# Optimization experiments

Hardware: AMD Instinct MI355X
Metric: run time of the kernel (lower is better)

The kernel has to match this reference:

```python
import jax, jax.numpy as jnp
import numpy as np

MARGIN = 70.0
THR = 125.0
PD_EPS = 1e-6  # torch F.pairwise_distance default eps


def _return_cam(features, weight_softmax, class_idx):
    # features: [bz, nc, h, w]; weight_softmax: [n_cls, nc]; class_idx: [bz]
    w_sel = weight_softmax[class_idx]                     # [bz, nc]
    cam = jnp.einsum('bc,bchw->bhw', w_sel, features)     # [bz, h, w]
    cam = cam - cam.min(axis=(1, 2), keepdims=True)
    cam = cam / cam.max(axis=(1, 2), keepdims=True) * 255.0
    return cam[:, None]                                   # [bz, 1, h, w]


def _pairwise_distance(x, y):
    # torch F.pairwise_distance: ||x - y + eps||_2 along last dim
    return jnp.sqrt(jnp.sum((x - y + PD_EPS) ** 2, axis=-1))


def setup_inputs() -> dict:
    key = jax.random.key(0)
    ks = jax.random.split(key, 6)
    bz, nc, h, w, n_cls = 64, 2048, 14, 14, 1000
    return {
        'pred': jax.random.normal(ks[0], (bz, n_cls), jnp.float32),
        'cla_truth': jax.random.randint(ks[1], (bz,), 0, n_cls, jnp.int32),
        'seg_truth': jax.random.uniform(ks[2], (bz, h, w), jnp.float32),
        'features_blobs': jax.random.normal(ks[3], (bz, nc, h, w), jnp.float32),
        'weight_softmax': jax.random.normal(ks[4], (n_cls, nc), jnp.float32),
        'idx': jax.random.randint(ks[5], (bz, 3), 0, n_cls, jnp.int32),
    }


def reference(pred, cla_truth, seg_truth, features_blobs, weight_softmax, idx):
    bz, nc, h, w = features_blobs.shape
    # cross entropy
    logp = jax.nn.log_softmax(pred, axis=-1)
    loss1 = -jnp.mean(logp[jnp.arange(bz), cla_truth])
    # CAMs for top-3 predicted classes
    cam0 = _return_cam(features_blobs, weight_softmax, idx[:, 0])  # [bz,1,h,w]
    cam1 = _return_cam(features_blobs, weight_softmax, idx[:, 1])
    cam2 = _return_cam(features_blobs, weight_softmax, idx[:, 2])
    # binarize cam0 (values in [0,255]); <=thr -> 0, >thr -> 1
    dst = jnp.where(cam0[:, 0] > THR, 1.0, 0.0)                     # [bz,h,w]
    # row-wise distance to seg truth, averaged over rows
    ed1 = jnp.mean(_pairwise_distance(dst, seg_truth), axis=1)      # [bz]
    # CAM-weighted features via broadcasted matmul (requires h == w)
    fea0 = jnp.matmul(cam0, features_blobs)                         # [bz,nc,h,w]
    fea1 = jnp.matmul(cam1, features_blobs)
    fea2 = jnp.matmul(cam2, features_blobs)
    d01 = _pairwise_distance(fea0.reshape(bz, -1), fea1.reshape(bz, -1)) / nc
    d02 = _pairwise_distance(fea0.reshape(bz, -1), fea2.reshape(bz, -1)) / nc
    loss_dis = jnp.mean(ed1 + jnp.clip(MARGIN - d01 - d02, 0.0, None)) + loss1
    return loss_dis
```

## Files before the change

kernel.cpp:

```cpp
#include <hip/hip_runtime.h>
#include <hip/hip_bf16.h>
#include <math.h>

#define BZ      64
#define NC      2048
#define HH      14
#define HW      196
#define NCLS    1000
#define SPLITS  8
#define CPB     (NC/SPLITS)
#define CHUNK   8
#define NCHUNK  (CPB/CHUNK)

#define CAM_OFF  0
#define G_OFF    (BZ*SPLITS*3*HW)
#define S_OFF    (G_OFF + BZ*SPLITS*HW)
#define TERM_OFF (S_OFF + BZ*SPLITS*HH)

__global__ __launch_bounds__(320) void k_stage1(
    const float* __restrict__ F, const float* __restrict__ W,
    const int* __restrict__ idx, float* __restrict__ ws)
{
  __shared__ __align__(16) float Fs[2][CHUNK*HW];
  __shared__ __align__(16) float wls[3][CPB];
  __shared__ __align__(16) float sred[HW];
  __shared__ __align__(16) float gred[224*4];

  const int t = threadIdx.x;
  const int s = blockIdx.x;
  const int b = blockIdx.y;
  const int cbase = s*CPB;

  const int i0 = idx[b*3+0], i1 = idx[b*3+1], i2 = idx[b*3+2];
  if (t < CPB){
    wls[0][t] = W[(size_t)i0*NC + cbase + t];
    wls[1][t] = W[(size_t)i1*NC + cbase + t];
    wls[2][t] = W[(size_t)i2*NC + cbase + t];
  }

  const float* Fb = F + ((size_t)b*NC + cbase)*HW;

  const bool isCam = (t < 49);
  const bool isG   = (t >= 64 && t < 288);
  int m0=0,m1=0,n0=0,n1=0, cg=0, tmKeep=0, tnKeep=0;
  if (isG){
    int g = t - 64;
    int tile = g % 28; cg = g / 28;
    int k = tile, tm = 0;
    while (k >= 7 - tm){ k -= 7 - tm; tm++; }
    int tn = tm + k;
    tmKeep = tm; tnKeep = tn;
    m0 = 2*tm; m1 = m0+1; n0 = 2*tn; n1 = n0+1;
  }
  (void)tmKeep; (void)tnKeep;

  float4 c0a = make_float4(0.f,0.f,0.f,0.f);
  float4 c1a = make_float4(0.f,0.f,0.f,0.f);
  float4 c2a = make_float4(0.f,0.f,0.f,0.f);
  float4 sA  = make_float4(0.f,0.f,0.f,0.f);
  float g00=0.f, g01=0.f, g10=0.f, g11=0.f;

  float4 pre0 = make_float4(0.f,0.f,0.f,0.f);
  float4 pre1 = make_float4(0.f,0.f,0.f,0.f);

  auto loadChunk = [&](int ch){
    if (t < 196){
      const float4* src = (const float4*)(Fb + (size_t)ch*CHUNK*HW);
      pre0 = src[2*t]; pre1 = src[2*t+1];
    }
  };
  auto storeChunk = [&](int bufi){
    if (t < 196){
      float4* dst = (float4*)(&Fs[bufi][0]);
      dst[2*t] = pre0; dst[2*t+1] = pre1;
    }
  };

  loadChunk(0);
  storeChunk(0);
  __syncthreads();

  for (int ch = 0; ch < NCHUNK; ++ch){
    const int bufi = ch & 1;
    if (ch+1 < NCHUNK) loadChunk(ch+1);
    const float* Fsb = &Fs[bufi][0];

    if (isCam){
      float w0a[CHUNK], w1a[CHUNK], w2a[CHUNK];
      *(float4*)&w0a[0] = *(const float4*)&wls[0][ch*CHUNK];
      *(float4*)&w0a[4] = *(const float4*)&wls[0][ch*CHUNK+4];
      *(float4*)&w1a[0] = *(const float4*)&wls[1][ch*CHUNK];
      *(float4*)&w1a[4] = *(const float4*)&wls[1][ch*CHUNK+4];
      *(float4*)&w2a[0] = *(const float4*)&wls[2][ch*CHUNK];
      *(float4*)&w2a[4] = *(const float4*)&wls[2][ch*CHUNK+4];
      #pragma unroll
      for (int c=0;c<CHUNK;c++){
        float4 v = *(const float4*)(Fsb + c*HW + 4*t);
        c0a.x += w0a[c]*v.x; c0a.y += w0a[c]*v.y; c0a.z += w0a[c]*v.z; c0a.w += w0a[c]*v.w;
        c1a.x += w1a[c]*v.x; c1a.y += w1a[c]*v.y; c1a.z += w1a[c]*v.z; c1a.w += w1a[c]*v.w;
        c2a.x += w2a[c]*v.x; c2a.y += w2a[c]*v.y; c2a.z += w2a[c]*v.z; c2a.w += w2a[c]*v.w;
        sA.x += v.x; sA.y += v.y; sA.z += v.z; sA.w += v.w;
      }
    }
    if (isG){
      const float* Mb = Fsb + cg*HW;
      const float2* r0 = (const float2*)(Mb + m0*HH);
      const float2* r1 = (const float2*)(Mb + m1*HH);
      const float2* q0 = (const float2*)(Mb + n0*HH);
      const float2* q1 = (const float2*)(Mb + n1*HH);
      #pragma unroll
      for (int jj=0;jj<7;jj++){
        float2 a0=r0[jj], a1=r1[jj], b0=q0[jj], b1=q1[jj];
        g00 += a0.x*b0.x + a0.y*b0.y;
        g01 += a0.x*b1.x + a0.y*b1.y;
        g10 += a1.x*b0.x + a1.y*b0.y;
        g11 += a1.x*b1.x + a1.y*b1.y;
      }
    }
    if (ch+1 < NCHUNK) storeChunk((ch+1)&1);
    __syncthreads();
  }

  const size_t pslot = (size_t)(b*SPLITS + s);
  if (isCam){
    float* base = ws + CAM_OFF + pslot*3*HW;
    *(float4*)(base          + 4*t) = c0a;
    *(float4*)(base + HW     + 4*t) = c1a;
    *(float4*)(base + 2*HW   + 4*t) = c2a;
    *(float4*)(sred + 4*t) = sA;
  }
  if (isG){
    int g = t - 64;
    float* gr = &gred[g*4];
    gr[0]=g00; gr[1]=g01; gr[2]=g10; gr[3]=g11;
  }
  __syncthreads();

  if (t < HH){
    float acc=0.f;
    #pragma unroll
    for (int j=0;j<HH;j++) acc += sred[t*HH+j];
    ws[S_OFF + pslot*HH + t] = acc;
  }
  if (t < 112){
    int tile = t >> 2, q = t & 3;
    int k = tile, tm2 = 0;
    while (k >= 7 - tm2){ k -= 7 - tm2; tm2++; }
    int tn2 = tm2 + k;
    float acc=0.f;
    #pragma unroll
    for (int c=0;c<8;c++) acc += gred[(c*28+tile)*4 + q];
    int a = q>>1, bb = q&1;
    int mm = 2*tm2 + a, nn = 2*tn2 + bb;
    float* gb = ws + G_OFF + pslot*HW;
    gb[mm*HH+nn] = acc;
    if (tn2 > tm2) gb[nn*HH+mm] = acc;
  }
}

template<int MODE>
__device__ __forceinline__ float bred(float v, float* red){
  #pragma unroll
  for (int o=32;o>0;o>>=1){
    float u = __shfl_down(v, o, 64);
    if (MODE==0) v += u; else if (MODE==1) v = fminf(v,u); else v = fmaxf(v,u);
  }
  __syncthreads();
  if ((threadIdx.x & 63)==0) red[threadIdx.x>>6] = v;
  __syncthreads();
  float r = red[0];
  #pragma unroll
  for (int w=1;w<4;w++){
    float u = red[w];
    if (MODE==0) r += u; else if (MODE==1) r = fminf(r,u); else r = fmaxf(r,u);
  }
  return r;
}

__global__ __launch_bounds__(256) void k_stage2(
    const float* __restrict__ pred, const int* __restrict__ cla,
    const float* __restrict__ seg, float* __restrict__ ws)
{
  const int t = threadIdx.x, b = blockIdx.x;
  __shared__ float cam[3][HW], Gm[HW], Sv[HH];
  __shared__ float D1[HW], D2[HW], EE[HW];
  __shared__ float rowv[HH], dc1[HH], dc2[HH];
  __shared__ float red[4];
  __shared__ float scal[6];

  if (t < HW){
    for (int k=0;k<3;k++){
      float a=0.f;
      for (int s=0;s<SPLITS;s++)
        a += ws[CAM_OFF + ((size_t)(b*SPLITS+s)*3 + k)*HW + t];
      cam[k][t]=a;
    }
    float g=0.f;
    for (int s=0;s<SPLITS;s++) g += ws[G_OFF + (size_t)(b*SPLITS+s)*HW + t];
    Gm[t]=g;
  }
  if (t < HH){
    float a=0.f;
    for (int s=0;s<SPLITS;s++) a += ws[S_OFF + (size_t)(b*SPLITS+s)*HH + t];
    Sv[t]=a;
  }
  __syncthreads();

  for (int k=0;k<3;k++){
    float v = (t<HW)? cam[k][t] : 3.0e38f;
    float mn = bred<1>(v, red);
    v = (t<HW)? cam[k][t] : -3.0e38f;
    float mx = bred<2>(v, red);
    if (t==0){ scal[2*k]=mn; scal[2*k+1]=mx; }
  }
  __syncthreads();

  if (t < HW){
    float c0 = (cam[0][t]-scal[0]) / (scal[1]-scal[0]) * 255.0f;
    float c1 = (cam[1][t]-scal[2]) / (scal[3]-scal[2]) * 255.0f;
    float c2 = (cam[2][t]-scal[4]) / (scal[5]-scal[4]) * 255.0f;
    float dst = (c0 > 125.0f) ? 1.0f : 0.0f;
    D1[t] = c0 - c1; D2[t] = c0 - c2;
    float e = dst - seg[(size_t)b*HW + t] + 1e-6f;
    EE[t] = e*e;
  }
  __syncthreads();

  if (t < HH){
    float rs=0.f, d1=0.f, d2=0.f;
    #pragma unroll
    for (int j=0;j<HH;j++){
      rs += EE[t*HH+j];
      d1 += D1[j*HH+t];
      d2 += D2[j*HH+t];
    }
    rowv[t] = sqrtf(rs); dc1[t]=d1; dc2[t]=d2;
  }
  __syncthreads();

  float v1=0.f, v2=0.f;
  if (t < HW){
    int m = t/HH, mp = t%HH;
    float h1=0.f, h2=0.f;
    #pragma unroll
    for (int i=0;i<HH;i++){
      h1 += D1[i*HH+m]*D1[i*HH+mp];
      h2 += D2[i*HH+m]*D2[i*HH+mp];
    }
    v1 = h1*Gm[t]; v2 = h2*Gm[t];
  }
  float sx2_1 = bred<0>(v1, red);
  float sx2_2 = bred<0>(v2, red);

  const float* pb = pred + (size_t)b*NCLS;
  float mv = -3.0e38f;
  for (int i=t;i<NCLS;i+=256) mv = fmaxf(mv, pb[i]);
  mv = bred<2>(mv, red);
  float es = 0.f;
  for (int i=t;i<NCLS;i+=256) es += expf(pb[i]-mv);
  es = bred<0>(es, red);

  if (t==0){
    float lse = mv + logf(es);
    float ce  = lse - pb[cla[b]];
    float ed1 = 0.f;
    #pragma unroll
    for (int i=0;i<HH;i++) ed1 += rowv[i];
    ed1 *= (1.0f/14.0f);
    float sx1=0.f, sx2=0.f;
    #pragma unroll
    for (int m=0;m<HH;m++){ sx1 += dc1[m]*Sv[m]; sx2 += dc2[m]*Sv[m]; }
    const float NEPS2 = 401408.0f * 1e-12f;
    float d01 = sqrtf(sx2_1 + 2e-6f*sx1 + NEPS2) * (1.0f/2048.0f);
    float d02 = sqrtf(sx2_2 + 2e-6f*sx2 + NEPS2) * (1.0f/2048.0f);
    float term = ed1 + fmaxf(0.0f, 70.0f - d01 - d02) + ce;
    ws[TERM_OFF + b] = term;
  }
}

__global__ void k_stage3(const float* __restrict__ ws, float* __restrict__ out){
  float v = ws[TERM_OFF + threadIdx.x];
  #pragma unroll
  for (int o=32;o>0;o>>=1) v += __shfl_down(v, o, 64);
  if (threadIdx.x==0) out[0] = v * (1.0f/64.0f);
}

extern "C" void kernel_launch(void* const* d_in, const int* in_sizes, int n_in,
                              void* d_out, int out_size, void* d_ws, size_t ws_size,
                              hipStream_t stream) {
  const float* pred = (const float*)d_in[0];
  const int*   cla  = (const int*)  d_in[1];
  const float* seg  = (const float*)d_in[2];
  const float* F    = (const float*)d_in[3];
  const float* W    = (const float*)d_in[4];
  const int*   idx  = (const int*)  d_in[5];
  float* out = (float*)d_out;
  float* ws  = (float*)d_ws;

  dim3 g1(SPLITS, BZ);
  k_stage1<<<g1, 320, 0, stream>>>(F, W, idx, ws);
  k_stage2<<<BZ, 256, 0, stream>>>(pred, cla, seg, ws);
  k_stage3<<<1, 64, 0, stream>>>(ws, out);
}
```

Baseline: 179.7 us.

## Compute Gram matrix with per-column register accumulators over upper triangle

Restructures the Gram-matrix computation in stage 1. Each of 112 threads now owns one (channel, column) pair, loads the 14-element column into registers and accumulates all 105 upper-triangle products in registers. This replaces the previous scheme of 2x2 tiles of full-row dot products. Blocks shrink to 192 threads, the shared feature tile is padded to 200 floats per channel, and stage 2 reads the packed triangle. The cost is about 105 accumulator registers per thread plus a serial 112-way shared-memory reduction at the end, which risks lower occupancy.

```diff
diff --git a/kernel.cpp b/kernel.cpp
--- a/kernel.cpp
+++ b/kernel.cpp
@@ -1,5 +1,4 @@
 #include <hip/hip_runtime.h>
-#include <hip/hip_bf16.h>
 #include <math.h>
 
 #define BZ      64
@@ -11,20 +10,22 @@
 #define CPB     (NC/SPLITS)
 #define CHUNK   8
 #define NCHUNK  (CPB/CHUNK)
+#define LPAD    200
+#define NTRI    105
 
 #define CAM_OFF  0
 #define G_OFF    (BZ*SPLITS*3*HW)
 #define S_OFF    (G_OFF + BZ*SPLITS*HW)
 #define TERM_OFF (S_OFF + BZ*SPLITS*HH)
 
-__global__ __launch_bounds__(320) void k_stage1(
+__global__ __launch_bounds__(192) void k_stage1(
     const float* __restrict__ F, const float* __restrict__ W,
     const int* __restrict__ idx, float* __restrict__ ws)
 {
-  __shared__ __align__(16) float Fs[2][CHUNK*HW];
+  __shared__ __align__(16) float Fs[2][CHUNK*LPAD];
   __shared__ __align__(16) float wls[3][CPB];
   __shared__ __align__(16) float sred[HW];
-  __shared__ __align__(16) float gred[224*4];
+  __shared__ __align__(16) float gacc[112*NTRI];
 
   const int t = threadIdx.x;
   const int s = blockIdx.x;
@@ -32,59 +33,65 @@
   const int cbase = s*CPB;
 
   const int i0 = idx[b*3+0], i1 = idx[b*3+1], i2 = idx[b*3+2];
-  if (t < CPB){
-    wls[0][t] = W[(size_t)i0*NC + cbase + t];
-    wls[1][t] = W[(size_t)i1*NC + cbase + t];
-    wls[2][t] = W[(size_t)i2*NC + cbase + t];
+  for (int i = t; i < CPB; i += 192){
+    wls[0][i] = W[(size_t)i0*NC + cbase + i];
+    wls[1][i] = W[(size_t)i1*NC + cbase + i];
+    wls[2][i] = W[(size_t)i2*NC + cbase + i];
   }
 
   const float* Fb = F + ((size_t)b*NC + cbase)*HW;
 
-  const bool isCam = (t < 49);
-  const bool isG   = (t >= 64 && t < 288);
-  int m0=0,m1=0,n0=0,n1=0, cg=0, tmKeep=0, tnKeep=0;
-  if (isG){
-    int g = t - 64;
-    int tile = g % 28; cg = g / 28;
-    int k = tile, tm = 0;
-    while (k >= 7 - tm){ k -= 7 - tm; tm++; }
-    int tn = tm + k;
-    tmKeep = tm; tnKeep = tn;
-    m0 = 2*tm; m1 = m0+1; n0 = 2*tn; n1 = n0+1;
-  }
-  (void)tmKeep; (void)tnKeep;
-
+  const bool isG   = (t < 112);
+  const int  cL    = t & 7;
+  const int  jc    = t >> 3;
+  const bool isCam = (t >= 128 && t < 177);
+  const int  cp    = t - 128;
+
+  float acc[NTRI];
+  #pragma unroll
+  for (int k=0;k<NTRI;k++) acc[k]=0.f;
   float4 c0a = make_float4(0.f,0.f,0.f,0.f);
   float4 c1a = make_float4(0.f,0.f,0.f,0.f);
   float4 c2a = make_float4(0.f,0.f,0.f,0.f);
   float4 sA  = make_float4(0.f,0.f,0.f,0.f);
-  float g00=0.f, g01=0.f, g10=0.f, g11=0.f;
-
-  float4 pre0 = make_float4(0.f,0.f,0.f,0.f);
-  float4 pre1 = make_float4(0.f,0.f,0.f,0.f);
-
+
+  float4 p0, p1, p2;
   auto loadChunk = [&](int ch){
-    if (t < 196){
-      const float4* src = (const float4*)(Fb + (size_t)ch*CHUNK*HW);
-      pre0 = src[2*t]; pre1 = src[2*t+1];
-    }
+    const float4* src = (const float4*)(Fb + (size_t)ch*CHUNK*HW);
+    p0 = src[t];
+    p1 = src[t+192];
+    if (t < 8) p2 = src[t+384];
   };
   auto storeChunk = [&](int bufi){
-    if (t < 196){
-      float4* dst = (float4*)(&Fs[bufi][0]);
-      dst[2*t] = pre0; dst[2*t+1] = pre1;
-    }
+    float4* dst = (float4*)(&Fs[bufi][0]);
+    int i = t;       dst[(i/49)*(LPAD/4) + (i%49)] = p0;
+    i = t + 192;     dst[(i/49)*(LPAD/4) + (i%49)] = p1;
+    if (t < 8){ i = t + 384; dst[(i/49)*(LPAD/4) + (i%49)] = p2; }
   };
 
   loadChunk(0);
   storeChunk(0);
   __syncthreads();
 
+  #pragma unroll 1
   for (int ch = 0; ch < NCHUNK; ++ch){
     const int bufi = ch & 1;
     if (ch+1 < NCHUNK) loadChunk(ch+1);
     const float* Fsb = &Fs[bufi][0];
 
+    if (isG){
+      const float* colp = Fsb + cL*LPAD + jc;
+      float x[14];
+      #pragma unroll
+      for (int m=0;m<14;m++) x[m] = colp[m*HH];
+      #pragma unroll
+      for (int m=0;m<14;m++){
+        #pragma unroll
+        for (int n=m;n<14;n++){
+          acc[14*m - (m*(m-1))/2 + (n-m)] += x[m]*x[n];
+        }
+      }
+    }
     if (isCam){
       float w0a[CHUNK], w1a[CHUNK], w2a[CHUNK];
       *(float4*)&w0a[0] = *(const float4*)&wls[0][ch*CHUNK];
@@ -95,28 +102,13 @@
       *(float4*)&w2a[4] = *(const float4*)&wls[2][ch*CHUNK+4];
       #pragma unroll
       for (int c=0;c<CHUNK;c++){
-        float4 v = *(const float4*)(Fsb + c*HW + 4*t);
+        float4 v = *(const float4*)(Fsb + c*LPAD + 4*cp);
         c0a.x += w0a[c]*v.x; c0a.y += w0a[c]*v.y; c0a.z += w0a[c]*v.z; c0a.w += w0a[c]*v.w;
         c1a.x += w1a[c]*v.x; c1a.y += w1a[c]*v.y; c1a.z += w1a[c]*v.z; c1a.w += w1a[c]*v.w;
         c2a.x += w2a[c]*v.x; c2a.y += w2a[c]*v.y; c2a.z += w2a[c]*v.z; c2a.w += w2a[c]*v.w;
         sA.x += v.x; sA.y += v.y; sA.z += v.z; sA.w += v.w;
       }
     }
-    if (isG){
-      const float* Mb = Fsb + cg*HW;
-      const float2* r0 = (const float2*)(Mb + m0*HH);
-      const float2* r1 = (const float2*)(Mb + m1*HH);
-      const float2* q0 = (const float2*)(Mb + n0*HH);
-      const float2* q1 = (const float2*)(Mb + n1*HH);
-      #pragma unroll
-      for (int jj=0;jj<7;jj++){
-        float2 a0=r0[jj], a1=r1[jj], b0=q0[jj], b1=q1[jj];
-        g00 += a0.x*b0.x + a0.y*b0.y;
-        g01 += a0.x*b1.x + a0.y*b1.y;
-        g10 += a1.x*b0.x + a1.y*b0.y;
-        g11 += a1.x*b1.x + a1.y*b1.y;
-      }
-    }
     if (ch+1 < NCHUNK) storeChunk((ch+1)&1);
     __syncthreads();
   }
@@ -124,37 +116,29 @@
   const size_t pslot = (size_t)(b*SPLITS + s);
   if (isCam){
     float* base = ws + CAM_OFF + pslot*3*HW;
-    *(float4*)(base          + 4*t) = c0a;
-    *(float4*)(base + HW     + 4*t) = c1a;
-    *(float4*)(base + 2*HW   + 4*t) = c2a;
-    *(float4*)(sred + 4*t) = sA;
+    *(float4*)(base          + 4*cp) = c0a;
+    *(float4*)(base + HW     + 4*cp) = c1a;
+    *(float4*)(base + 2*HW   + 4*cp) = c2a;
+    *(float4*)(sred + 4*cp) = sA;
   }
   if (isG){
-    int g = t - 64;
-    float* gr = &gred[g*4];
-    gr[0]=g00; gr[1]=g01; gr[2]=g10; gr[3]=g11;
-  }
-  __syncthreads();
-
-  if (t < HH){
-    float acc=0.f;
-    #pragma unroll
-    for (int j=0;j<HH;j++) acc += sred[t*HH+j];
-    ws[S_OFF + pslot*HH + t] = acc;
-  }
-  if (t < 112){
-    int tile = t >> 2, q = t & 3;
-    int k = tile, tm2 = 0;
-    while (k >= 7 - tm2){ k -= 7 - tm2; tm2++; }
-    int tn2 = tm2 + k;
-    float acc=0.f;
-    #pragma unroll
-    for (int c=0;c<8;c++) acc += gred[(c*28+tile)*4 + q];
-    int a = q>>1, bb = q&1;
-    int mm = 2*tm2 + a, nn = 2*tn2 + bb;
-    float* gb = ws + G_OFF + pslot*HW;
-    gb[mm*HH+nn] = acc;
-    if (tn2 > tm2) gb[nn*HH+mm] = acc;
+    float* gr = &gacc[t*NTRI];
+    #pragma unroll
+    for (int k=0;k<NTRI;k++) gr[k] = acc[k];
+  }
+  __syncthreads();
+
+  if (t < NTRI){
+    float a = 0.f;
+    for (int th=0; th<112; th++) a += gacc[th*NTRI + t];
+    ws[G_OFF + pslot*HW + t] = a;
+  }
+  if (t >= 128 && t < 128+HH){
+    int r = t - 128;
+    float a = 0.f;
+    #pragma unroll
+    for (int j=0;j<HH;j++) a += sred[r*HH+j];
+    ws[S_OFF + pslot*HH + r] = a;
   }
 }
 
@@ -182,7 +166,7 @@
     const float* __restrict__ seg, float* __restrict__ ws)
 {
   const int t = threadIdx.x, b = blockIdx.x;
-  __shared__ float cam[3][HW], Gm[HW], Sv[HH];
+  __shared__ float cam[3][HW], Gt[NTRI], Sv[HH];
   __shared__ float D1[HW], D2[HW], EE[HW];
   __shared__ float rowv[HH], dc1[HH], dc2[HH];
   __shared__ float red[4];
@@ -195,9 +179,11 @@
         a += ws[CAM_OFF + ((size_t)(b*SPLITS+s)*3 + k)*HW + t];
       cam[k][t]=a;
     }
+  }
+  if (t < NTRI){
     float g=0.f;
     for (int s=0;s<SPLITS;s++) g += ws[G_OFF + (size_t)(b*SPLITS+s)*HW + t];
-    Gm[t]=g;
+    Gt[t]=g;
   }
   if (t < HH){
     float a=0.f;
@@ -247,7 +233,9 @@
       h1 += D1[i*HH+m]*D1[i*HH+mp];
       h2 += D2[i*HH+m]*D2[i*HH+mp];
     }
-    v1 = h1*Gm[t]; v2 = h2*Gm[t];
+    int mm = (m<mp)?m:mp, nn = (m<mp)?mp:m;
+    float g = Gt[14*mm - (mm*(mm-1))/2 + (nn-mm)];
+    v1 = h1*g; v2 = h2*g;
   }
   float sx2_1 = bred<0>(v1, red);
   float sx2_2 = bred<0>(v2, red);
@@ -298,7 +286,7 @@
   float* ws  = (float*)d_ws;
 
   dim3 g1(SPLITS, BZ);
-  k_stage1<<<g1, 320, 0, stream>>>(F, W, idx, ws);
+  k_stage1<<<g1, 192, 0, stream>>>(F, W, idx, ws);
   k_stage2<<<BZ, 256, 0, stream>>>(pred, cla, seg, ws);
   k_stage3<<<1, 64, 0, stream>>>(ws, out);
 }
```

After: 180.3 us. No clear change (+0.4%).
